# Kernel optimization log

Measured on AMD Instinct MI355X. Metric: run time of the kernel, lower is better.

## Reference

```python
import jax, jax.numpy as jnp
import numpy as np

IN_DIM = 1024
LOW_D_FF = 128
OUT_DIM = 1024
B = 8
S = 2048

def _xavier_normal(key, shape):
    fan_in, fan_out = shape[1], shape[0]
    std = float(np.sqrt(2.0 / (fan_in + fan_out)))
    return jax.random.normal(key, shape, dtype=jnp.float32) * std

def setup_inputs() -> dict:
    key = jax.random.key(0)
    kx, kk, kd, ku = jax.random.split(key, 4)
    x = jax.random.normal(kx, (B, S, IN_DIM), dtype=jnp.float32)
    k = jax.random.normal(kk, (B, LOW_D_FF), dtype=jnp.float32)
    D_matrix = _xavier_normal(kd, (IN_DIM * LOW_D_FF, LOW_D_FF))
    U_matrix = _xavier_normal(ku, (LOW_D_FF * OUT_DIM, LOW_D_FF))
    return {"x": x, "k": k, "D_matrix": D_matrix, "U_matrix": U_matrix}

def reference(x, k, D_matrix, U_matrix):
    # x: [B, S, in_dim], k: [B, low_d_ff]
    Bn = x.shape[0]
    low = k.shape[-1]
    # hypernetwork weight generation: per-sample D [B, in_dim, low], U [B, low, out_dim]
    D = jnp.einsum('pk,bk->bp', D_matrix, k).reshape(Bn, IN_DIM, low)
    U = jnp.einsum('pk,bk->bp', U_matrix, k).reshape(Bn, low, OUT_DIM)
    h = jax.nn.relu(jnp.einsum('bsd,bdl->bsl', x, D))
    return jnp.einsum('bsl,blo->bso', h, U)
```

## Files before the change

kernel.cpp:

```cpp
#include <hip/hip_runtime.h>
#include <hip/hip_bf16.h>
#include <stdint.h>

#define IN_DIM  1024
#define LOW     128
#define OUT_DIM 1024
#define BATCH   8
#define SEQ     2048

typedef unsigned short u16;
typedef short bf16x8 __attribute__((ext_vector_type(8)));
typedef unsigned short u16x4 __attribute__((ext_vector_type(4)));
typedef float f32x4 __attribute__((ext_vector_type(4)));

__device__ __forceinline__ u16 f2bf(float f) {
    union { float f; uint32_t u; } v;
    v.f = f;
    uint32_t u = v.u;
    return (u16)((u + 0x7fffu + ((u >> 16) & 1u)) >> 16);
}

__global__ __launch_bounds__(256) void gen_w(const float* __restrict__ Dm,
                                             const float* __restrict__ Um,
                                             const float* __restrict__ kv,
                                             u16* __restrict__ DgT,
                                             u16* __restrict__ UgT) {
    __shared__ float stage[16 * 128];
    __shared__ u16 tb[BATCH * 8 * 32];

    int t = threadIdx.x;
    int bid = blockIdx.x;
    bool isU = bid >= 512;
    int rb = isU ? (bid - 512) : bid;
    const float* src = isU ? Um : Dm;
    u16* out = isU ? UgT : DgT;
    int NTOT = isU ? 1024 : 128;
    int MTOT = isU ? 128 : 1024;
    int sh = isU ? 7 : 4;
    int m0 = (rb >> sh) * 32;
    int n0 = (rb & ((1 << sh) - 1)) * 8;

    int r  = t >> 4;
    int bp = (t >> 2) & 3;
    int q  = t & 3;
    int sw = ((q << 1) ^ (r & 7)) & 7;

    f32x4 kr0[8], kr1[8];
#pragma unroll
    for (int j4 = 0; j4 < 8; ++j4) {
        kr0[j4] = *(const f32x4*)(kv + (2 * bp)     * LOW + q * 32 + j4 * 4);
        kr1[j4] = *(const f32x4*)(kv + (2 * bp + 1) * LOW + q * 32 + j4 * 4);
    }

    for (int ch = 0; ch < 16; ++ch) {
        __syncthreads();
#pragma unroll
        for (int i = 0; i < 2; ++i) {
            int f = t + 256 * i;
            int rs = f >> 5, c = f & 31;
            int qs = c >> 3, j4s = c & 7;
            int cp = (qs << 3) | (j4s ^ (((qs << 1) ^ (rs & 7)) & 7));
            int m = m0 + 2 * ch + (rs >> 3);
            int n = n0 + (rs & 7);
            f32x4 v = *(const f32x4*)(src + ((size_t)m * NTOT + n) * 128 + c * 4);
            *(f32x4*)(stage + rs * 128 + cp * 4) = v;
        }
        __syncthreads();
        float a0 = 0.f, a1 = 0.f;
#pragma unroll
        for (int j4 = 0; j4 < 8; ++j4) {
            f32x4 a = *(const f32x4*)(stage + r * 128 + ((q << 3) | (j4 ^ sw)) * 4);
            a0 += a.x * kr0[j4].x + a.y * kr0[j4].y + a.z * kr0[j4].z + a.w * kr0[j4].w;
            a1 += a.x * kr1[j4].x + a.y * kr1[j4].y + a.z * kr1[j4].z + a.w * kr1[j4].w;
        }
        a0 += __shfl_xor(a0, 1); a0 += __shfl_xor(a0, 2);
        a1 += __shfl_xor(a1, 1); a1 += __shfl_xor(a1, 2);
        if (q == 0) {
            int nn = r & 7, mm = 2 * ch + (r >> 3);
            tb[(2 * bp)     * 256 + nn * 32 + mm] = f2bf(a0);
            tb[(2 * bp + 1) * 256 + nn * 32 + mm] = f2bf(a1);
        }
    }
    __syncthreads();
    int c64 = t >> 2, q4 = t & 3;
    int bw = c64 >> 3, np = c64 & 7;
    bf16x8 v = *(const bf16x8*)(tb + bw * 256 + np * 32 + q4 * 8);
    *(bf16x8*)(out + ((size_t)(bw * NTOT + n0 + np)) * MTOT + m0 + q4 * 8) = v;
}

__global__ __launch_bounds__(256) void fc1(const float* __restrict__ x,
                                           const u16* __restrict__ DgT,
                                           u16* __restrict__ h) {
    __shared__ u16 As[32][72];
    __shared__ u16 Bs[128][72];
    int t = threadIdx.x;
    int bid = blockIdx.x;
    int b = bid >> 6, st = bid & 63;
    int s0 = st * 32;
    const float* xb = x + ((size_t)b * SEQ + s0) * IN_DIM;
    const u16* Db = DgT + (size_t)b * LOW * IN_DIM;

    int w = t >> 6, lane = t & 63;
    int wm = w >> 1, wn = w & 1;
    int lr = lane & 15, hi = lane >> 4;

    f32x4 acc[4];
#pragma unroll
    for (int nf = 0; nf < 4; ++nf) acc[nf] = (f32x4){0.f, 0.f, 0.f, 0.f};

    int ar = t >> 3, ac = t & 7;
    int brt = t >> 3, bc = t & 7;

    for (int kt = 0; kt < IN_DIM / 64; ++kt) {
        int k0 = kt * 64;
#pragma unroll
        for (int i = 0; i < 2; ++i) {
            float4 v = *(const float4*)(xb + (size_t)ar * IN_DIM + k0 + ac * 4 + i * 32);
            u16x4 o;
            o.x = f2bf(v.x); o.y = f2bf(v.y); o.z = f2bf(v.z); o.w = f2bf(v.w);
            *(u16x4*)(&As[ar][ac * 4 + i * 32]) = o;
        }
#pragma unroll
        for (int i = 0; i < 4; ++i) {
            int row = brt + 32 * i;
            bf16x8 v = *(const bf16x8*)(Db + (size_t)row * IN_DIM + k0 + bc * 8);
            *(bf16x8*)(&Bs[row][bc * 8]) = v;
        }
        __syncthreads();
#pragma unroll
        for (int ks = 0; ks < 2; ++ks) {
            int kk = ks * 32 + hi * 8;
            bf16x8 af = *(const bf16x8*)(&As[wm * 16 + lr][kk]);
#pragma unroll
            for (int nf = 0; nf < 4; ++nf) {
                bf16x8 bf = *(const bf16x8*)(&Bs[wn * 64 + nf * 16 + lr][kk]);
                acc[nf] = __builtin_amdgcn_mfma_f32_16x16x32_bf16(af, bf, acc[nf], 0, 0, 0);
            }
        }
        __syncthreads();
    }
    u16* hb = h + ((size_t)b * SEQ + s0) * LOW;
#pragma unroll
    for (int nf = 0; nf < 4; ++nf) {
        int col = wn * 64 + nf * 16 + lr;
#pragma unroll
        for (int j = 0; j < 4; ++j) {
            int rrow = wm * 16 + hi * 4 + j;
            hb[(size_t)rrow * LOW + col] = f2bf(fmaxf(acc[nf][j], 0.f));
        }
    }
}

__global__ __launch_bounds__(256) void fc2(const u16* __restrict__ h,
                                           const u16* __restrict__ UgT,
                                           float* __restrict__ out) {
    __shared__ u16 As[128 * 128];
    __shared__ u16 Bs[128 * 128];
    int t = threadIdx.x;
    int bid = blockIdx.x;
    int b = bid >> 7, st = (bid >> 3) & 15, ot = bid & 7;
    int s0 = st * 128, o0 = ot * 128;
    const u16* hb = h + ((size_t)b * SEQ + s0) * LOW;
    const u16* Ub = UgT + ((size_t)b * OUT_DIM + o0) * LOW;

#pragma unroll
    for (int i = 0; i < 8; ++i) {
        int ch = i * 256 + t;
        int row = ch >> 4, c = ch & 15;
        int swc = c ^ (row & 7);
        *(bf16x8*)(As + row * 128 + swc * 8) = *(const bf16x8*)(hb + (size_t)ch * 8);
        *(bf16x8*)(Bs + row * 128 + swc * 8) = *(const bf16x8*)(Ub + (size_t)ch * 8);
    }
    __syncthreads();

    int w = t >> 6, lane = t & 63;
    int wm = w >> 1, wn = w & 1;
    int lr = lane & 15, lkc = (lane >> 4);

    f32x4 acc[4][4];
#pragma unroll
    for (int mf = 0; mf < 4; ++mf)
#pragma unroll
        for (int nf = 0; nf < 4; ++nf)
            acc[mf][nf] = (f32x4){0.f, 0.f, 0.f, 0.f};

#pragma unroll
    for (int ks = 0; ks < 4; ++ks) {
        bf16x8 af[4], bfr[4];
#pragma unroll
        for (int mf = 0; mf < 4; ++mf) {
            int row = wm * 64 + mf * 16 + lr;
            int swc = (ks * 4 + lkc) ^ (row & 7);
            af[mf] = *(const bf16x8*)(As + row * 128 + swc * 8);
        }
#pragma unroll
        for (int nf = 0; nf < 4; ++nf) {
            int row = wn * 64 + nf * 16 + lr;
            int swc = (ks * 4 + lkc) ^ (row & 7);
            bfr[nf] = *(const bf16x8*)(Bs + row * 128 + swc * 8);
        }
#pragma unroll
        for (int mf = 0; mf < 4; ++mf)
#pragma unroll
            for (int nf = 0; nf < 4; ++nf)
                acc[mf][nf] = __builtin_amdgcn_mfma_f32_16x16x32_bf16(
                    af[mf], bfr[nf], acc[mf][nf], 0, 0, 0);
    }

    float* ob = out + ((size_t)b * SEQ + s0) * OUT_DIM + o0;
#pragma unroll
    for (int mf = 0; mf < 4; ++mf)
#pragma unroll
        for (int nf = 0; nf < 4; ++nf) {
            int col = wn * 64 + nf * 16 + lr;
#pragma unroll
            for (int j = 0; j < 4; ++j) {
                int rrow = wm * 64 + mf * 16 + (lane >> 4) * 4 + j;
                ob[(size_t)rrow * OUT_DIM + col] = acc[mf][nf][j];
            }
        }
}

extern "C" void kernel_launch(void* const* d_in, const int* in_sizes, int n_in,
                              void* d_out, int out_size, void* d_ws, size_t ws_size,
                              hipStream_t stream) {
    const float* x  = (const float*)d_in[0];
    const float* kv = (const float*)d_in[1];
    const float* Dm = (const float*)d_in[2];
    const float* Um = (const float*)d_in[3];
    float* out = (float*)d_out;

    u16* DgT = (u16*)d_ws;
    u16* UgT = DgT + (size_t)BATCH * LOW * IN_DIM;
    u16* hbuf = UgT + (size_t)BATCH * OUT_DIM * LOW;

    gen_w<<<dim3(1024), dim3(256), 0, stream>>>(Dm, Um, kv, DgT, UgT);
    fc1<<<dim3(512), dim3(256), 0, stream>>>(x, DgT, hbuf);
    fc2<<<dim3(1024), dim3(256), 0, stream>>>(hbuf, UgT, out);
}
```

Baseline: 71.56 us.

## Double-buffer gen_w staging and halve per-block m-tile to double block count

The weight-generation kernel now keeps two LDS stage buffers. It prefetches the next chunk's global loads into registers while the current chunk is reduced, which removes one barrier per iteration. Each block now covers 16 m rows instead of 32, so the grid grows from 1024 to 2048 blocks for more parallelism in this bandwidth-bound stage. The cost is narrower 8-byte output stores and more per-block setup overhead.

```diff
diff --git a/kernel.cpp b/kernel.cpp
--- a/kernel.cpp
+++ b/kernel.cpp
@@ -25,20 +25,31 @@
                                              const float* __restrict__ kv,
                                              u16* __restrict__ DgT,
                                              u16* __restrict__ UgT) {
-    __shared__ float stage[16 * 128];
-    __shared__ u16 tb[BATCH * 8 * 32];
+    __shared__ float stage[2][16 * 128];
+    __shared__ u16 tb[BATCH * 8 * 16];
 
     int t = threadIdx.x;
     int bid = blockIdx.x;
-    bool isU = bid >= 512;
-    int rb = isU ? (bid - 512) : bid;
+    bool isU = bid >= 1024;
+    int rb = isU ? (bid - 1024) : bid;
     const float* src = isU ? Um : Dm;
-    u16* out = isU ? UgT : DgT;
+    u16* outp = isU ? UgT : DgT;
     int NTOT = isU ? 1024 : 128;
     int MTOT = isU ? 128 : 1024;
     int sh = isU ? 7 : 4;
-    int m0 = (rb >> sh) * 32;
+    int m0 = (rb >> sh) * 16;
     int n0 = (rb & ((1 << sh) - 1)) * 8;
+
+    int rs0 = t >> 5, c0 = t & 31;
+    int rs1 = rs0 + 8;
+    int qs0 = c0 >> 3, j4s0 = c0 & 7;
+    int cp0 = (qs0 << 3) | (j4s0 ^ (((qs0 << 1) ^ (rs0 & 7)) & 7));
+    int cp1 = (qs0 << 3) | (j4s0 ^ (((qs0 << 1) ^ (rs1 & 7)) & 7));
+    int so0 = rs0 * 128 + cp0 * 4;
+    int so1 = rs1 * 128 + cp1 * 4;
+    const float* g0 = src + ((size_t)(m0 + 0) * NTOT + n0 + (rs0 & 7)) * 128 + c0 * 4;
+    const float* g1 = src + ((size_t)(m0 + 1) * NTOT + n0 + (rs1 & 7)) * 128 + c0 * 4;
+    size_t gstride = (size_t)2 * NTOT * 128;
 
     int r  = t >> 4;
     int bp = (t >> 2) & 3;
@@ -52,24 +63,23 @@
         kr1[j4] = *(const f32x4*)(kv + (2 * bp + 1) * LOW + q * 32 + j4 * 4);
     }
 
-    for (int ch = 0; ch < 16; ++ch) {
-        __syncthreads();
-#pragma unroll
-        for (int i = 0; i < 2; ++i) {
-            int f = t + 256 * i;
-            int rs = f >> 5, c = f & 31;
-            int qs = c >> 3, j4s = c & 7;
-            int cp = (qs << 3) | (j4s ^ (((qs << 1) ^ (rs & 7)) & 7));
-            int m = m0 + 2 * ch + (rs >> 3);
-            int n = n0 + (rs & 7);
-            f32x4 v = *(const f32x4*)(src + ((size_t)m * NTOT + n) * 128 + c * 4);
-            *(f32x4*)(stage + rs * 128 + cp * 4) = v;
-        }
-        __syncthreads();
+    f32x4 v0 = *(const f32x4*)g0;
+    f32x4 v1 = *(const f32x4*)g1;
+    *(f32x4*)(stage[0] + so0) = v0;
+    *(f32x4*)(stage[0] + so1) = v1;
+    __syncthreads();
+
+    for (int ch = 0; ch < 8; ++ch) {
+        int cur = ch & 1;
+        if (ch < 7) {
+            v0 = *(const f32x4*)(g0 + (size_t)(ch + 1) * gstride);
+            v1 = *(const f32x4*)(g1 + (size_t)(ch + 1) * gstride);
+        }
         float a0 = 0.f, a1 = 0.f;
+        const float* sb = stage[cur] + r * 128;
 #pragma unroll
         for (int j4 = 0; j4 < 8; ++j4) {
-            f32x4 a = *(const f32x4*)(stage + r * 128 + ((q << 3) | (j4 ^ sw)) * 4);
+            f32x4 a = *(const f32x4*)(sb + ((q << 3) | (j4 ^ sw)) * 4);
             a0 += a.x * kr0[j4].x + a.y * kr0[j4].y + a.z * kr0[j4].z + a.w * kr0[j4].w;
             a1 += a.x * kr1[j4].x + a.y * kr1[j4].y + a.z * kr1[j4].z + a.w * kr1[j4].w;
         }
@@ -77,15 +87,20 @@
         a1 += __shfl_xor(a1, 1); a1 += __shfl_xor(a1, 2);
         if (q == 0) {
             int nn = r & 7, mm = 2 * ch + (r >> 3);
-            tb[(2 * bp)     * 256 + nn * 32 + mm] = f2bf(a0);
-            tb[(2 * bp + 1) * 256 + nn * 32 + mm] = f2bf(a1);
-        }
-    }
-    __syncthreads();
-    int c64 = t >> 2, q4 = t & 3;
-    int bw = c64 >> 3, np = c64 & 7;
-    bf16x8 v = *(const bf16x8*)(tb + bw * 256 + np * 32 + q4 * 8);
-    *(bf16x8*)(out + ((size_t)(bw * NTOT + n0 + np)) * MTOT + m0 + q4 * 8) = v;
+            tb[(2 * bp)     * 128 + nn * 16 + mm] = f2bf(a0);
+            tb[(2 * bp + 1) * 128 + nn * 16 + mm] = f2bf(a1);
+        }
+        if (ch < 7) {
+            *(f32x4*)(stage[cur ^ 1] + so0) = v0;
+            *(f32x4*)(stage[cur ^ 1] + so1) = v1;
+        }
+        __syncthreads();
+    }
+
+    int pair = t >> 2, sub = t & 3;
+    int bw = pair >> 3, np = pair & 7;
+    u16x4 v = *(const u16x4*)(tb + bw * 128 + np * 16 + sub * 4);
+    *(u16x4*)(outp + ((size_t)(bw * NTOT + n0 + np)) * MTOT + m0 + sub * 4) = v;
 }
 
 __global__ __launch_bounds__(256) void fc1(const float* __restrict__ x,
@@ -234,7 +249,7 @@
     u16* UgT = DgT + (size_t)BATCH * LOW * IN_DIM;
     u16* hbuf = UgT + (size_t)BATCH * OUT_DIM * LOW;
 
-    gen_w<<<dim3(1024), dim3(256), 0, stream>>>(Dm, Um, kv, DgT, UgT);
+    gen_w<<<dim3(2048), dim3(256), 0, stream>>>(Dm, Um, kv, DgT, UgT);
     fc1<<<dim3(512), dim3(256), 0, stream>>>(x, DgT, hbuf);
     fc2<<<dim3(1024), dim3(256), 0, stream>>>(hbuf, UgT, out);
 }
```

New measurement: 71.87 us. Within noise of the previous version (+0.4%).

## Double-buffer gen_w loads via global_load_lds and contract with bf16 MFMA

Applied to the files above, without the earlier changes.

The weight-generation kernel is restructured. It now streams the hypernetwork matrices straight into LDS with async global_load_lds, double-buffered in 64-row chunks, so the next chunk's loads overlap the current chunk's compute. The scalar FMA dot products and shuffle reductions are replaced by 16x16x32 bf16 MFMA, with k held as a B fragment padded from 8 to 16 columns. The large fp32 source matrices are rounded to bf16 before the contraction, which loses some precision. Correctness also depends on the compiler waiting for the async LDS loads before each barrier.

```diff
diff --git a/kernel.cpp b/kernel.cpp
--- a/kernel.cpp
+++ b/kernel.cpp
@@ -20,72 +20,96 @@
     return (u16)((u + 0x7fffu + ((u >> 16) & 1u)) >> 16);
 }
 
+__device__ __forceinline__ void gload16(const float* g, float* l) {
+    __builtin_amdgcn_global_load_lds(
+        (const __attribute__((address_space(1))) void*)g,
+        (__attribute__((address_space(3))) void*)l, 16, 0, 0);
+}
+
 __global__ __launch_bounds__(256) void gen_w(const float* __restrict__ Dm,
                                              const float* __restrict__ Um,
                                              const float* __restrict__ kv,
                                              u16* __restrict__ DgT,
                                              u16* __restrict__ UgT) {
-    __shared__ float stage[16 * 128];
-    __shared__ u16 tb[BATCH * 8 * 32];
+    __shared__ float sbuf[2][64 * 128];
+    __shared__ u16 tb[8 * 8 * 32];
 
     int t = threadIdx.x;
     int bid = blockIdx.x;
     bool isU = bid >= 512;
     int rb = isU ? (bid - 512) : bid;
     const float* src = isU ? Um : Dm;
-    u16* out = isU ? UgT : DgT;
+    u16* outp = isU ? UgT : DgT;
     int NTOT = isU ? 1024 : 128;
     int MTOT = isU ? 128 : 1024;
     int sh = isU ? 7 : 4;
     int m0 = (rb >> sh) * 32;
     int n0 = (rb & ((1 << sh) - 1)) * 8;
 
-    int r  = t >> 4;
-    int bp = (t >> 2) & 3;
-    int q  = t & 3;
-    int sw = ((q << 1) ^ (r & 7)) & 7;
-
-    f32x4 kr0[8], kr1[8];
-#pragma unroll
-    for (int j4 = 0; j4 < 8; ++j4) {
-        kr0[j4] = *(const f32x4*)(kv + (2 * bp)     * LOW + q * 32 + j4 * 4);
-        kr1[j4] = *(const f32x4*)(kv + (2 * bp + 1) * LOW + q * 32 + j4 * 4);
-    }
-
-    for (int ch = 0; ch < 16; ++ch) {
+    int g8 = t >> 5;
+    int srcChunk = (t & 31) ^ g8;
+    const float* gbase = src + ((size_t)m0 * NTOT + n0 + g8) * 128 + srcChunk * 4;
+    size_t mstep = (size_t)NTOT * 128;
+
+    int lane = t & 63, w = t >> 6;
+    int bb = lane & 15;
+    int hi = lane >> 4;
+    int rsw = lane & 7;
+
+    bf16x8 bfrag[4];
+#pragma unroll
+    for (int ks = 0; ks < 4; ++ks)
+#pragma unroll
+        for (int j = 0; j < 8; ++j) {
+            float kvf = (bb < 8) ? kv[bb * LOW + ks * 32 + hi * 8 + j] : 0.f;
+            bfrag[ks][j] = (short)f2bf(kvf);
+        }
+
+    {
+        float* l0 = &sbuf[0][t * 4];
+#pragma unroll
+        for (int i = 0; i < 8; ++i)
+            gload16(gbase + (size_t)i * mstep, l0 + i * 1024);
+    }
+
+    for (int c = 0; c < 4; ++c) {
         __syncthreads();
-#pragma unroll
-        for (int i = 0; i < 2; ++i) {
-            int f = t + 256 * i;
-            int rs = f >> 5, c = f & 31;
-            int qs = c >> 3, j4s = c & 7;
-            int cp = (qs << 3) | (j4s ^ (((qs << 1) ^ (rs & 7)) & 7));
-            int m = m0 + 2 * ch + (rs >> 3);
-            int n = n0 + (rs & 7);
-            f32x4 v = *(const f32x4*)(src + ((size_t)m * NTOT + n) * 128 + c * 4);
-            *(f32x4*)(stage + rs * 128 + cp * 4) = v;
-        }
-        __syncthreads();
-        float a0 = 0.f, a1 = 0.f;
-#pragma unroll
-        for (int j4 = 0; j4 < 8; ++j4) {
-            f32x4 a = *(const f32x4*)(stage + r * 128 + ((q << 3) | (j4 ^ sw)) * 4);
-            a0 += a.x * kr0[j4].x + a.y * kr0[j4].y + a.z * kr0[j4].z + a.w * kr0[j4].w;
-            a1 += a.x * kr1[j4].x + a.y * kr1[j4].y + a.z * kr1[j4].z + a.w * kr1[j4].w;
-        }
-        a0 += __shfl_xor(a0, 1); a0 += __shfl_xor(a0, 2);
-        a1 += __shfl_xor(a1, 1); a1 += __shfl_xor(a1, 2);
-        if (q == 0) {
-            int nn = r & 7, mm = 2 * ch + (r >> 3);
-            tb[(2 * bp)     * 256 + nn * 32 + mm] = f2bf(a0);
-            tb[(2 * bp + 1) * 256 + nn * 32 + mm] = f2bf(a1);
+        if (c < 3) {
+            float* ln = &sbuf[(c + 1) & 1][t * 4];
+            const float* gn = gbase + (size_t)(8 * (c + 1)) * mstep;
+#pragma unroll
+            for (int i = 0; i < 8; ++i)
+                gload16(gn + (size_t)i * mstep, ln + i * 1024);
+        }
+        const float* rowp = sbuf[c & 1] + (w * 16 + bb) * 128;
+        f32x4 acc = (f32x4){0.f, 0.f, 0.f, 0.f};
+#pragma unroll
+        for (int ks = 0; ks < 4; ++ks) {
+            int c0 = ks * 8 + hi * 2;
+            f32x4 v0 = *(const f32x4*)(rowp + ((c0)     ^ rsw) * 4);
+            f32x4 v1 = *(const f32x4*)(rowp + ((c0 + 1) ^ rsw) * 4);
+            bf16x8 afr;
+            afr[0] = (short)f2bf(v0.x); afr[1] = (short)f2bf(v0.y);
+            afr[2] = (short)f2bf(v0.z); afr[3] = (short)f2bf(v0.w);
+            afr[4] = (short)f2bf(v1.x); afr[5] = (short)f2bf(v1.y);
+            afr[6] = (short)f2bf(v1.z); afr[7] = (short)f2bf(v1.w);
+            acc = __builtin_amdgcn_mfma_f32_16x16x32_bf16(afr, bfrag[ks], acc, 0, 0, 0);
+        }
+        if (bb < 8) {
+#pragma unroll
+            for (int j = 0; j < 4; ++j) {
+                int r = hi * 4 + j;
+                int mm = c * 8 + w * 2 + (r >> 3);
+                tb[bb * 256 + (r & 7) * 32 + mm] = f2bf(acc[j]);
+            }
         }
     }
     __syncthreads();
+
     int c64 = t >> 2, q4 = t & 3;
     int bw = c64 >> 3, np = c64 & 7;
     bf16x8 v = *(const bf16x8*)(tb + bw * 256 + np * 32 + q4 * 8);
-    *(bf16x8*)(out + ((size_t)(bw * NTOT + n0 + np)) * MTOT + m0 + q4 * 8) = v;
+    *(bf16x8*)(outp + ((size_t)(bw * NTOT + n0 + np)) * MTOT + m0 + q4 * 8) = v;
 }
 
 __global__ __launch_bounds__(256) void fc1(const float* __restrict__ x,
```

New measurement: 71.39 us. About the same (-0.2%).

## Rewrite hypernetwork weight generation to use register-direct loads and wave shuffles

Applied to the files above, without the earlier changes.

The weight-generation kernel no longer stages the D/U matrices through LDS in 16 sequential chunks with barriers. Each wave now loads four rows of 8x128 floats straight into registers, dots them against all 8 batch k vectors, and reduces across 32 lanes with xor shuffles. Tiles are halved to 16 m-rows and the grid is doubled to 2048 blocks, which exposes more memory-level parallelism for the streaming read of the large matrices. In exchange it performs many more shuffles (8 batches times 5 steps per element) and narrower 8-byte output stores.

```diff
diff --git a/kernel.cpp b/kernel.cpp
--- a/kernel.cpp
+++ b/kernel.cpp
@@ -25,67 +25,66 @@
                                              const float* __restrict__ kv,
                                              u16* __restrict__ DgT,
                                              u16* __restrict__ UgT) {
-    __shared__ float stage[16 * 128];
-    __shared__ u16 tb[BATCH * 8 * 32];
+    __shared__ u16 tb[8 * 8 * 16];
 
     int t = threadIdx.x;
     int bid = blockIdx.x;
-    bool isU = bid >= 512;
-    int rb = isU ? (bid - 512) : bid;
+    bool isU = bid >= 1024;
+    int rb = isU ? (bid - 1024) : bid;
     const float* src = isU ? Um : Dm;
-    u16* out = isU ? UgT : DgT;
+    u16* outp = isU ? UgT : DgT;
     int NTOT = isU ? 1024 : 128;
     int MTOT = isU ? 128 : 1024;
     int sh = isU ? 7 : 4;
-    int m0 = (rb >> sh) * 32;
+    int m0 = (rb >> sh) * 16;
     int n0 = (rb & ((1 << sh) - 1)) * 8;
 
-    int r  = t >> 4;
-    int bp = (t >> 2) & 3;
-    int q  = t & 3;
-    int sw = ((q << 1) ^ (r & 7)) & 7;
-
-    f32x4 kr0[8], kr1[8];
-#pragma unroll
-    for (int j4 = 0; j4 < 8; ++j4) {
-        kr0[j4] = *(const f32x4*)(kv + (2 * bp)     * LOW + q * 32 + j4 * 4);
-        kr1[j4] = *(const f32x4*)(kv + (2 * bp + 1) * LOW + q * 32 + j4 * 4);
-    }
-
-    for (int ch = 0; ch < 16; ++ch) {
-        __syncthreads();
-#pragma unroll
-        for (int i = 0; i < 2; ++i) {
-            int f = t + 256 * i;
-            int rs = f >> 5, c = f & 31;
-            int qs = c >> 3, j4s = c & 7;
-            int cp = (qs << 3) | (j4s ^ (((qs << 1) ^ (rs & 7)) & 7));
-            int m = m0 + 2 * ch + (rs >> 3);
-            int n = n0 + (rs & 7);
-            f32x4 v = *(const f32x4*)(src + ((size_t)m * NTOT + n) * 128 + c * 4);
-            *(f32x4*)(stage + rs * 128 + cp * 4) = v;
-        }
-        __syncthreads();
-        float a0 = 0.f, a1 = 0.f;
-#pragma unroll
-        for (int j4 = 0; j4 < 8; ++j4) {
-            f32x4 a = *(const f32x4*)(stage + r * 128 + ((q << 3) | (j4 ^ sw)) * 4);
-            a0 += a.x * kr0[j4].x + a.y * kr0[j4].y + a.z * kr0[j4].z + a.w * kr0[j4].w;
-            a1 += a.x * kr1[j4].x + a.y * kr1[j4].y + a.z * kr1[j4].z + a.w * kr1[j4].w;
-        }
-        a0 += __shfl_xor(a0, 1); a0 += __shfl_xor(a0, 2);
-        a1 += __shfl_xor(a1, 1); a1 += __shfl_xor(a1, 2);
-        if (q == 0) {
-            int nn = r & 7, mm = 2 * ch + (r >> 3);
-            tb[(2 * bp)     * 256 + nn * 32 + mm] = f2bf(a0);
-            tb[(2 * bp + 1) * 256 + nn * 32 + mm] = f2bf(a1);
+    int w = t >> 6, lane = t & 63;
+    int q = lane & 31, h = lane >> 5;
+
+    f32x4 kq[8];
+#pragma unroll
+    for (int b = 0; b < 8; ++b)
+        kq[b] = *(const f32x4*)(kv + b * LOW + q * 4);
+
+    f32x4 L[4][4];
+#pragma unroll
+    for (int mj = 0; mj < 4; ++mj) {
+        int m = m0 + w * 4 + mj;
+        const float* bp = src + ((size_t)m * NTOT + n0) * 128 + lane * 4;
+#pragma unroll
+        for (int j = 0; j < 4; ++j)
+            L[mj][j] = *(const f32x4*)(bp + j * 256);
+    }
+
+#pragma unroll
+    for (int mj = 0; mj < 4; ++mj) {
+        int mloc = w * 4 + mj;
+#pragma unroll
+        for (int j = 0; j < 4; ++j) {
+            f32x4 v = L[mj][j];
+            float a[8];
+#pragma unroll
+            for (int b = 0; b < 8; ++b)
+                a[b] = v.x * kq[b].x + v.y * kq[b].y + v.z * kq[b].z + v.w * kq[b].w;
+#pragma unroll
+            for (int s = 1; s <= 16; s <<= 1)
+#pragma unroll
+                for (int b = 0; b < 8; ++b)
+                    a[b] += __shfl_xor(a[b], s);
+            int nl = 2 * j + h;
+#pragma unroll
+            for (int b = 0; b < 8; ++b)
+                if (q == b)
+                    tb[b * 128 + nl * 16 + mloc] = f2bf(a[b]);
         }
     }
     __syncthreads();
-    int c64 = t >> 2, q4 = t & 3;
-    int bw = c64 >> 3, np = c64 & 7;
-    bf16x8 v = *(const bf16x8*)(tb + bw * 256 + np * 32 + q4 * 8);
-    *(bf16x8*)(out + ((size_t)(bw * NTOT + n0 + np)) * MTOT + m0 + q4 * 8) = v;
+
+    int pair = t >> 2, q4 = t & 3;
+    int bw = pair >> 3, np = pair & 7;
+    u16x4 vv = *(const u16x4*)(tb + bw * 128 + np * 16 + q4 * 4);
+    *(u16x4*)(outp + ((size_t)(bw * NTOT + n0 + np)) * MTOT + m0 + q4 * 4) = vv;
 }
 
 __global__ __launch_bounds__(256) void fc1(const float* __restrict__ x,
@@ -234,7 +233,7 @@
     u16* UgT = DgT + (size_t)BATCH * LOW * IN_DIM;
     u16* hbuf = UgT + (size_t)BATCH * OUT_DIM * LOW;
 
-    gen_w<<<dim3(1024), dim3(256), 0, stream>>>(Dm, Um, kv, DgT, UgT);
+    gen_w<<<dim3(2048), dim3(256), 0, stream>>>(Dm, Um, kv, DgT, UgT);
     fc1<<<dim3(512), dim3(256), 0, stream>>>(x, DgT, hbuf);
     fc2<<<dim3(1024), dim3(256), 0, stream>>>(hbuf, UgT, out);
 }
```

New measurement: 108.7 us. 51.9% more time.
